# Kernel optimization log

Hardware: AMD Instinct MI355X
Metric: run time of the kernel (lower is better)

## Reference

```python
import jax, jax.numpy as jnp
import numpy as np

N_NODES = 50000
N_EDGES = 500000
IN_DIM = 64
OUT_DIM = 64
NUM_RELS = 16


def setup_inputs() -> dict:
    key = jax.random.key(0)
    ks = jax.random.split(key, 8)
    h = jax.random.normal(ks[0], (N_NODES, IN_DIM), dtype=jnp.float32)
    he = jax.random.normal(ks[1], (N_EDGES, IN_DIM), dtype=jnp.float32)
    src = jax.random.randint(ks[2], (N_EDGES,), 0, N_NODES)
    dst = jax.random.randint(ks[3], (N_EDGES,), 0, N_NODES)
    rel = jax.random.randint(ks[4], (N_EDGES,), 0, NUM_RELS)
    # xavier-ish scales
    W_shared = jax.random.normal(ks[5], (OUT_DIM, IN_DIM), dtype=jnp.float32) * (2.0 / (IN_DIM + OUT_DIM)) ** 0.5
    W_attn = jax.random.normal(ks[6], (1, 3 * OUT_DIM), dtype=jnp.float32) * (2.0 / (3 * OUT_DIM + 1)) ** 0.5
    W_rel = jax.random.normal(ks[7], (NUM_RELS, IN_DIM, OUT_DIM), dtype=jnp.float32) * (2.0 / (IN_DIM + OUT_DIM)) ** 0.5
    return {"h": h, "he": he, "src": src, "dst": dst, "rel": rel,
            "W_shared": W_shared, "W_attn": W_attn, "W_rel": W_rel}


def reference(h, he, src, dst, rel, W_shared, W_attn, W_rel):
    # --- edge attention: a = attn_fc([z_src, z_edge, z_dst]) (raw linear score, no softmax in original) ---
    Z = h @ W_shared.T                      # [N, out] project all nodes once
    ze = he @ W_shared.T                    # [E, out]
    # split attn weight to avoid materializing [E, 3*out] concat
    Wa_s, Wa_e, Wa_d = jnp.split(W_attn, 3, axis=1)   # each [1, out]
    a = Z[src] @ Wa_s.T + ze @ Wa_e.T + Z[dst] @ Wa_d.T   # [E, 1]
    # --- message: msg = (h_src @ W_rel[rel]) * a ---
    # compute per-(node, relation) transform once [N, R, out], then gather per edge
    H_all = jnp.einsum('ni,rio->nro', h, W_rel)          # [N, R, out]
    msg = H_all[src, rel] * a                             # [E, out]
    # --- scatter-sum aggregation into destination nodes ---
    out = jax.ops.segment_sum(msg, dst, num_segments=N_NODES)  # [N, out]
    # apply_func: activation (relu), no bias
    return jax.nn.relu(out)
```

## Files before the change

### kernel.cpp

```cpp
#include <hip/hip_runtime.h>
#include <math.h>

#define N_NODES 50000
#define N_EDGES 500000
#define NUM_RELS 16
#define GH 64
#define SCAN_BLKS 196
#define AE_BLKS 1954

typedef _Float16 f16x8 __attribute__((ext_vector_type(8)));
typedef _Float16 f16x4 __attribute__((ext_vector_type(4)));
typedef float    f32x4 __attribute__((ext_vector_type(4)));


__global__ void kz(int* __restrict__ c1, int* __restrict__ cu1,
                   int* __restrict__ c2, int* __restrict__ cu2) {
    int i = blockIdx.x * 256 + threadIdx.x;
    if (i < NUM_RELS) { c1[i] = 0; cu1[i] = 0; }
    if (i < N_NODES)  { c2[i] = 0; cu2[i] = 0; }
}

__global__ __launch_bounds__(256) void k_node(
    const float* __restrict__ h,
    const float* __restrict__ W_shared, const float* __restrict__ W_attn,
    const int* __restrict__ dst, const int* __restrict__ rel,
    float* __restrict__ sn, float* __restrict__ dn,
    int* __restrict__ c1, int* __restrict__ c2,
    _Float16* __restrict__ h_hi, _Float16* __restrict__ h_lo) {
    __shared__ float sus[64], sud[64];
    __shared__ int hist[NUM_RELS];
    const int t = threadIdx.x, bid = blockIdx.x, nb = gridDim.x;
    if (t < 64) {
        float us = 0.f, ud = 0.f;
        for (int o = 0; o < 64; ++o) {
            float w = W_shared[o * 64 + t];
            us = fmaf(w, W_attn[o],       us);
            ud = fmaf(w, W_attn[128 + o], ud);
        }
        sus[t] = us; sud[t] = ud;
    }
    if (t < NUM_RELS) hist[t] = 0;
    __syncthreads();

    int n = bid * 256 + t;
    if (n < N_NODES) {
        const float* hp = h + (size_t)n * 64;
        float s = 0.f, d = 0.f;
#pragma unroll
        for (int i = 0; i < 64; i += 4) {
            float4 v = *(const float4*)(hp + i);
            s = fmaf(v.x, sus[i], s);     s = fmaf(v.y, sus[i + 1], s);
            s = fmaf(v.z, sus[i + 2], s); s = fmaf(v.w, sus[i + 3], s);
            d = fmaf(v.x, sud[i], d);     d = fmaf(v.y, sud[i + 1], d);
            d = fmaf(v.z, sud[i + 2], d); d = fmaf(v.w, sud[i + 3], d);
            f16x4 hi, lo;
            hi[0] = (_Float16)v.x; lo[0] = (_Float16)(v.x - (float)hi[0]);
            hi[1] = (_Float16)v.y; lo[1] = (_Float16)(v.y - (float)hi[1]);
            hi[2] = (_Float16)v.z; lo[2] = (_Float16)(v.z - (float)hi[2]);
            hi[3] = (_Float16)v.w; lo[3] = (_Float16)(v.w - (float)hi[3]);
            *(f16x4*)(h_hi + (size_t)n * 64 + i) = hi;
            *(f16x4*)(h_lo + (size_t)n * 64 + i) = lo;
        }
        sn[n] = s; dn[n] = d;
    }
    for (int e = bid * 256 + t; e < N_EDGES; e += nb * 256) {
        atomicAdd(&hist[rel[e]], 1);
        atomicAdd(&c2[dst[e]], 1);
    }
    __syncthreads();
    if (t < NUM_RELS && hist[t]) atomicAdd(&c1[t], hist[t]);
}

__global__ __launch_bounds__(256) void k_scan1(const int* __restrict__ c2,
                                               int* __restrict__ partial) {
    const int t = threadIdx.x, bid = blockIdx.x;
    const int lane = t & 63, wv = t >> 6;
    __shared__ int ws[4];
    int idx = bid * 256 + t;
    int s = (idx < N_NODES) ? c2[idx] : 0;
#pragma unroll
    for (int off = 32; off > 0; off >>= 1) s += __shfl_xor(s, off, 64);
    if (lane == 0) ws[wv] = s;
    __syncthreads();
    if (t == 0) partial[bid] = ws[0] + ws[1] + ws[2] + ws[3];
}

__global__ __launch_bounds__(256) void k_scan2(const int* __restrict__ partial,
                                               int* __restrict__ pbase,
                                               int* __restrict__ offs2,
                                               const int* __restrict__ c1,
                                               int* __restrict__ offs1) {
    const int t = threadIdx.x;
    const int lane = t & 63, wv = t >> 6;
    __shared__ int wsum[4];
    int v = (t < SCAN_BLKS) ? partial[t] : 0;
    int x = v;
#pragma unroll
    for (int off = 1; off < 64; off <<= 1) {
        int y = __shfl_up(x, off, 64);
        if (lane >= off) x += y;
    }
    if (lane == 63) wsum[wv] = x;
    __syncthreads();
    int wbase = 0;
#pragma unroll
    for (int j = 0; j < 4; ++j) if (j < wv) wbase += wsum[j];
    int excl = wbase + x - v;
    pbase[t] = excl;
    if (t == 255) offs2[N_NODES] = excl;
    if (t == 0) {
        int b = 0;
        for (int r = 0; r < NUM_RELS; ++r) { offs1[r] = b; b += c1[r]; }
        offs1[NUM_RELS] = b;
    }
}

__global__ __launch_bounds__(256) void k_scan3(int* __restrict__ c2,
                                               const int* __restrict__ pbase,
                                               int* __restrict__ offs2) {
    const int t = threadIdx.x, bid = blockIdx.x;
    const int lane = t & 63, wv = t >> 6;
    __shared__ int wsum[4];
    int idx = bid * 256 + t;
    int v = (idx < N_NODES) ? c2[idx] : 0;
    int x = v;
#pragma unroll
    for (int off = 1; off < 64; off <<= 1) {
        int y = __shfl_up(x, off, 64);
        if (lane >= off) x += y;
    }
    if (lane == 63) wsum[wv] = x;
    __syncthreads();
    int wbase = 0;
#pragma unroll
    for (int j = 0; j < 4; ++j) if (j < wv) wbase += wsum[j];
    if (idx < N_NODES) offs2[idx] = pbase[bid] + wbase + x - v;
    if (idx < 4096) c2[idx] = 0;
}

__global__ __launch_bounds__(256) void k_ae(
    const float4* __restrict__ he4,
    const int* __restrict__ src, const int* __restrict__ dst,
    const int* __restrict__ rel,
    const float* __restrict__ W_shared, const float* __restrict__ W_attn,
    const float* __restrict__ sn, const float* __restrict__ dn,
    const int* __restrict__ offs1, int* __restrict__ cur1p,
    const int* __restrict__ offs2, int* __restrict__ cursor2,
    int* __restrict__ srcs, float* __restrict__ aes, int* __restrict__ iperm) {
    __shared__ float sve[64];
    __shared__ int hist[NUM_RELS], bbase[NUM_RELS], soffs[NUM_RELS];
    const int t = threadIdx.x;
    const int e = blockIdx.x * 256 + t;
    if (t < 64) {
        float ve = 0.f;
        for (int o = 0; o < 64; ++o)
            ve = fmaf(W_shared[o * 64 + t], W_attn[64 + o], ve);
        sve[t] = ve;
    }
    if (t < NUM_RELS) { hist[t] = 0; soffs[t] = offs1[t]; }
    const bool valid = (e < N_EDGES);
    int r = 0, s_ = 0, d_ = 0;
    float sdv = 0.f;
    if (valid) {
        s_ = src[e]; d_ = dst[e]; r = rel[e];
        sdv = sn[s_] + dn[d_];
    }
    __syncthreads();
    int lpos = 0; float aev = 0.f;
    if (valid) {
        const float4* hr = he4 + (size_t)e * 16;
        float acc = 0.f;
#pragma unroll
        for (int i = 0; i < 16; ++i) {
            float4 v = hr[i];
            float4 u = *(const float4*)(sve + 4 * i);
            acc += v.x * u.x + v.y * u.y + v.z * u.z + v.w * u.w;
        }
        aev = acc + sdv;
        lpos = atomicAdd(&hist[r], 1);
    }
    __syncthreads();
    if (t < NUM_RELS) bbase[t] = hist[t] ? atomicAdd(&cur1p[t << 8], hist[t]) : 0;
    __syncthreads();
    if (valid) {
        int p1 = soffs[r] + bbase[r] + lpos;
        srcs[p1] = s_; aes[p1] = aev;
        int p2 = offs2[d_] + atomicAdd(&cursor2[d_], 1);
        iperm[p2] = p1;
    }
}

__global__ __launch_bounds__(256, 4) void k_msg(
    const _Float16* __restrict__ h_hi, const _Float16* __restrict__ h_lo,
    const float* __restrict__ W_rel, const int* __restrict__ offs1,
    const int* __restrict__ srcs, const float* __restrict__ aes,
    float* __restrict__ msg)
{
    const int t = threadIdx.x;
    const int lane = t & 63;
    const int quad = lane >> 4;
    const int col  = lane & 15;
    const int wib  = t >> 6;
    const int rh   = blockIdx.x & 31;
    const int r    = rh & 15;
    const int half = rh >> 4;
    const int g    = blockIdx.x >> 5;
    const int wr   = g * 4 + wib;

    const int begin = __builtin_amdgcn_readfirstlane(offs1[r]);
    const int end   = __builtin_amdgcn_readfirstlane(offs1[r + 1]);

    const float* Wb = W_rel + (size_t)r * 4096;
    f16x8 bh[2][2], bl[2][2];
#pragma unroll
    for (int kb = 0; kb < 2; ++kb)
#pragma unroll
        for (int n2 = 0; n2 < 2; ++n2)
#pragma unroll
            for (int j = 0; j < 8; ++j) {
                float w = Wb[(kb * 32 + quad * 8 + j) * 64 + (half * 2 + n2) * 16 + col];
                _Float16 hi = (_Float16)w;
                bh[kb][n2][j] = hi;
                bl[kb][n2][j] = (_Float16)(w - (float)hi);
            }

    for (int base = begin + wr * 16; base < end; base += 256 * 16) {
        int m16 = end - base; if (m16 > 16) m16 = 16;
        const int ridx = base + (col < m16 ? col : m16 - 1);
        const int   sv = srcs[ridx];
        const float av = (col < m16) ? aes[ridx] : 0.f;

        const _Float16* ph = h_hi + (size_t)sv * 64 + quad * 8;
        const _Float16* pl = h_lo + (size_t)sv * 64 + quad * 8;
        f16x8 ah0 = *(const f16x8*)ph, ah1 = *(const f16x8*)(ph + 32);
        f16x8 al0 = *(const f16x8*)pl, al1 = *(const f16x8*)(pl + 32);

        f32x4 acc0 = {0.f, 0.f, 0.f, 0.f};
        f32x4 acc1 = {0.f, 0.f, 0.f, 0.f};
        acc0 = __builtin_amdgcn_mfma_f32_16x16x32_f16(ah0, bh[0][0], acc0, 0, 0, 0);
        acc1 = __builtin_amdgcn_mfma_f32_16x16x32_f16(ah0, bh[0][1], acc1, 0, 0, 0);
        acc0 = __builtin_amdgcn_mfma_f32_16x16x32_f16(ah0, bl[0][0], acc0, 0, 0, 0);
        acc1 = __builtin_amdgcn_mfma_f32_16x16x32_f16(ah0, bl[0][1], acc1, 0, 0, 0);
        acc0 = __builtin_amdgcn_mfma_f32_16x16x32_f16(al0, bh[0][0], acc0, 0, 0, 0);
        acc1 = __builtin_amdgcn_mfma_f32_16x16x32_f16(al0, bh[0][1], acc1, 0, 0, 0);
        acc0 = __builtin_amdgcn_mfma_f32_16x16x32_f16(ah1, bh[1][0], acc0, 0, 0, 0);
        acc1 = __builtin_amdgcn_mfma_f32_16x16x32_f16(ah1, bh[1][1], acc1, 0, 0, 0);
        acc0 = __builtin_amdgcn_mfma_f32_16x16x32_f16(ah1, bl[1][0], acc0, 0, 0, 0);
        acc1 = __builtin_amdgcn_mfma_f32_16x16x32_f16(ah1, bl[1][1], acc1, 0, 0, 0);
        acc0 = __builtin_amdgcn_mfma_f32_16x16x32_f16(al1, bh[1][0], acc0, 0, 0, 0);
        acc1 = __builtin_amdgcn_mfma_f32_16x16x32_f16(al1, bh[1][1], acc1, 0, 0, 0);

#pragma unroll
        for (int reg = 0; reg < 4; ++reg) {
            const int m = quad * 4 + reg;
            const float am = __shfl(av, m, 64);
            if (m < m16) {
                float* op = msg + (size_t)(base + m) * 64 + half * 32 + col;
                op[0]  = am * acc0[reg];
                op[16] = am * acc1[reg];
            }
        }
    }
}

__global__ __launch_bounds__(256) void k_out(
    const float* __restrict__ msg, const int* __restrict__ iperm,
    const int* __restrict__ offs2, float* __restrict__ out)
{
    const int lane = threadIdx.x & 63;
    const int gw   = blockIdx.x * 4 + (threadIdx.x >> 6);
    const int nw   = gridDim.x * 4;
    for (int n = gw; n < N_NODES; n += nw) {
        const int qb = offs2[n], qe = offs2[n + 1];
        float s0 = 0.f, s1 = 0.f, s2 = 0.f, s3 = 0.f;
        int q = qb;
        for (; q + 4 <= qe; q += 4) {
            int p0 = iperm[q], p1 = iperm[q + 1], p2 = iperm[q + 2], p3 = iperm[q + 3];
            s0 += msg[(size_t)p0 * 64 + lane];
            s1 += msg[(size_t)p1 * 64 + lane];
            s2 += msg[(size_t)p2 * 64 + lane];
            s3 += msg[(size_t)p3 * 64 + lane];
        }
        for (; q < qe; ++q)
            s0 += msg[(size_t)iperm[q] * 64 + lane];
        float s = (s0 + s1) + (s2 + s3);
        out[(size_t)n * 64 + lane] = fmaxf(s, 0.f);
    }
}

extern "C" void kernel_launch(void* const* d_in, const int* in_sizes, int n_in,
                              void* d_out, int out_size, void* d_ws, size_t ws_size,
                              hipStream_t stream) {
    const float*  h        = (const float*)d_in[0];
    const float4* he4      = (const float4*)d_in[1];
    const int*    src      = (const int*)d_in[2];
    const int*    dst      = (const int*)d_in[3];
    const int*    rel      = (const int*)d_in[4];
    const float*  W_shared = (const float*)d_in[5];
    const float*  W_attn   = (const float*)d_in[6];
    const float*  W_rel    = (const float*)d_in[7];
    float*        out      = (float*)d_out;

    int*      counts1 = (int*)d_ws + 0;
    int*      cursor1 = (int*)d_ws + 16;
    int*      offs1   = (int*)d_ws + 32;
    int*      counts2 = (int*)d_ws + 64;
    int*      cursor2 = (int*)d_ws + 50064;
    int*      offs2   = (int*)d_ws + 100064;
    float*    sn      = (float*)d_ws + 150080;
    float*    dn      = (float*)d_ws + 200080;
    int*      srcs    = (int*)d_ws + 250080;
    float*    aes     = (float*)d_ws + 750080;
    int*      iperm   = (int*)d_ws + 1250080;
    _Float16* h_hi    = (_Float16*)((int*)d_ws + 1750080);
    _Float16* h_lo    = (_Float16*)((int*)d_ws + 3350080);
    int*      partial = srcs;
    int*      pbase   = srcs + 256;
    float*    msg     = (float*)d_in[1];

    kz<<<(N_NODES + 255) / 256, 256, 0, stream>>>(counts1, cursor1, counts2, cursor2);
    k_node<<<196, 256, 0, stream>>>(h, W_shared, W_attn, dst, rel,
                                    sn, dn, counts1, counts2, h_hi, h_lo);
    k_scan1<<<SCAN_BLKS, 256, 0, stream>>>(counts2, partial);
    k_scan2<<<1, 256, 0, stream>>>(partial, pbase, offs2, counts1, offs1);
    k_scan3<<<SCAN_BLKS, 256, 0, stream>>>(counts2, pbase, offs2);
    k_ae<<<AE_BLKS, 256, 0, stream>>>(he4, src, dst, rel, W_shared, W_attn, sn, dn,
                                      offs1, counts2, offs2, cursor2, srcs, aes, iperm);
    k_msg<<<32 * GH, 256, 0, stream>>>(h_hi, h_lo, W_rel, offs1, srcs, aes, msg);
    k_out<<<2048, 256, 0, stream>>>(msg, iperm, offs2, out);
}
```

Baseline: 343.2 us.

## Coalesce edge-feature loads and scatter messages into destination order

k_ae now loads the edge-feature block cooperatively so consecutive lanes read consecutive float4s, computing per-edge dot products with shuffle reductions and shared memory. The permutation is inverted: k_msg writes each message directly to its destination-sorted slot, so k_out reads messages contiguously without an index gather. This trades gathered reads in the aggregation for scattered (but row-contiguous) writes in the message kernel, plus an extra perm load per edge.

```diff
diff --git a/kernel.cpp b/kernel.cpp
--- a/kernel.cpp
+++ b/kernel.cpp
@@ -146,11 +146,25 @@
     const float* __restrict__ sn, const float* __restrict__ dn,
     const int* __restrict__ offs1, int* __restrict__ cur1p,
     const int* __restrict__ offs2, int* __restrict__ cursor2,
-    int* __restrict__ srcs, float* __restrict__ aes, int* __restrict__ iperm) {
+    int* __restrict__ srcs, float* __restrict__ aes, int* __restrict__ perm) {
     __shared__ float sve[64];
+    __shared__ float sdot[256];
     __shared__ int hist[NUM_RELS], bbase[NUM_RELS], soffs[NUM_RELS];
     const int t = threadIdx.x;
+    const int lane = t & 63;
+    const int w = t >> 6;
     const int e = blockIdx.x * 256 + t;
+
+    const size_t fb = ((size_t)blockIdx.x * 256 + (size_t)w * 64) * 16;
+    const size_t fmax = (size_t)N_EDGES * 16 - 1;
+    float4 v[16];
+#pragma unroll
+    for (int k = 0; k < 16; ++k) {
+        size_t fi = fb + (size_t)k * 64 + lane;
+        if (fi > fmax) fi = fmax;
+        v[k] = he4[fi];
+    }
+
     if (t < 64) {
         float ve = 0.f;
         for (int o = 0; o < 64; ++o)
@@ -166,17 +180,22 @@
         sdv = sn[s_] + dn[d_];
     }
     __syncthreads();
+
+    {
+        float4 u = *(const float4*)(sve + 4 * (lane & 15));
+#pragma unroll
+        for (int k = 0; k < 16; ++k) {
+            float p = v[k].x * u.x + v[k].y * u.y + v[k].z * u.z + v[k].w * u.w;
+            p += __shfl_xor(p, 1, 64);
+            p += __shfl_xor(p, 2, 64);
+            p += __shfl_xor(p, 4, 64);
+            p += __shfl_xor(p, 8, 64);
+            if ((lane & 15) == 0) sdot[w * 64 + k * 4 + (lane >> 4)] = p;
+        }
+    }
     int lpos = 0; float aev = 0.f;
     if (valid) {
-        const float4* hr = he4 + (size_t)e * 16;
-        float acc = 0.f;
-#pragma unroll
-        for (int i = 0; i < 16; ++i) {
-            float4 v = hr[i];
-            float4 u = *(const float4*)(sve + 4 * i);
-            acc += v.x * u.x + v.y * u.y + v.z * u.z + v.w * u.w;
-        }
-        aev = acc + sdv;
+        aev = sdot[t] + sdv;
         lpos = atomicAdd(&hist[r], 1);
     }
     __syncthreads();
@@ -186,7 +205,7 @@
         int p1 = soffs[r] + bbase[r] + lpos;
         srcs[p1] = s_; aes[p1] = aev;
         int p2 = offs2[d_] + atomicAdd(&cursor2[d_], 1);
-        iperm[p2] = p1;
+        perm[p1] = p2;
     }
 }
 
@@ -194,7 +213,7 @@
     const _Float16* __restrict__ h_hi, const _Float16* __restrict__ h_lo,
     const float* __restrict__ W_rel, const int* __restrict__ offs1,
     const int* __restrict__ srcs, const float* __restrict__ aes,
-    float* __restrict__ msg)
+    const int* __restrict__ perm, float* __restrict__ msg)
 {
     const int t = threadIdx.x;
     const int lane = t & 63;
@@ -229,6 +248,7 @@
         const int ridx = base + (col < m16 ? col : m16 - 1);
         const int   sv = srcs[ridx];
         const float av = (col < m16) ? aes[ridx] : 0.f;
+        const int   pv = (col < m16) ? perm[ridx] : 0;
 
         const _Float16* ph = h_hi + (size_t)sv * 64 + quad * 8;
         const _Float16* pl = h_lo + (size_t)sv * 64 + quad * 8;
@@ -254,8 +274,9 @@
         for (int reg = 0; reg < 4; ++reg) {
             const int m = quad * 4 + reg;
             const float am = __shfl(av, m, 64);
+            const int   pm = __shfl(pv, m, 64);
             if (m < m16) {
-                float* op = msg + (size_t)(base + m) * 64 + half * 32 + col;
+                float* op = msg + (size_t)pm * 64 + half * 32 + col;
                 op[0]  = am * acc0[reg];
                 op[16] = am * acc1[reg];
             }
@@ -264,7 +285,7 @@
 }
 
 __global__ __launch_bounds__(256) void k_out(
-    const float* __restrict__ msg, const int* __restrict__ iperm,
+    const float* __restrict__ msg,
     const int* __restrict__ offs2, float* __restrict__ out)
 {
     const int lane = threadIdx.x & 63;
@@ -275,14 +296,13 @@
         float s0 = 0.f, s1 = 0.f, s2 = 0.f, s3 = 0.f;
         int q = qb;
         for (; q + 4 <= qe; q += 4) {
-            int p0 = iperm[q], p1 = iperm[q + 1], p2 = iperm[q + 2], p3 = iperm[q + 3];
-            s0 += msg[(size_t)p0 * 64 + lane];
-            s1 += msg[(size_t)p1 * 64 + lane];
-            s2 += msg[(size_t)p2 * 64 + lane];
-            s3 += msg[(size_t)p3 * 64 + lane];
+            s0 += msg[(size_t)q * 64 + lane];
+            s1 += msg[(size_t)(q + 1) * 64 + lane];
+            s2 += msg[(size_t)(q + 2) * 64 + lane];
+            s3 += msg[(size_t)(q + 3) * 64 + lane];
         }
         for (; q < qe; ++q)
-            s0 += msg[(size_t)iperm[q] * 64 + lane];
+            s0 += msg[(size_t)q * 64 + lane];
         float s = (s0 + s1) + (s2 + s3);
         out[(size_t)n * 64 + lane] = fmaxf(s, 0.f);
     }
@@ -311,7 +331,7 @@
     float*    dn      = (float*)d_ws + 200080;
     int*      srcs    = (int*)d_ws + 250080;
     float*    aes     = (float*)d_ws + 750080;
-    int*      iperm   = (int*)d_ws + 1250080;
+    int*      perm    = (int*)d_ws + 1250080;
     _Float16* h_hi    = (_Float16*)((int*)d_ws + 1750080);
     _Float16* h_lo    = (_Float16*)((int*)d_ws + 3350080);
     int*      partial = srcs;
@@ -325,7 +345,7 @@
     k_scan2<<<1, 256, 0, stream>>>(partial, pbase, offs2, counts1, offs1);
     k_scan3<<<SCAN_BLKS, 256, 0, stream>>>(counts2, pbase, offs2);
     k_ae<<<AE_BLKS, 256, 0, stream>>>(he4, src, dst, rel, W_shared, W_attn, sn, dn,
-                                      offs1, counts2, offs2, cursor2, srcs, aes, iperm);
-    k_msg<<<32 * GH, 256, 0, stream>>>(h_hi, h_lo, W_rel, offs1, srcs, aes, msg);
-    k_out<<<2048, 256, 0, stream>>>(msg, iperm, offs2, out);
-}
+                                      offs1, counts2, offs2, cursor2, srcs, aes, perm);
+    k_msg<<<32 * GH, 256, 0, stream>>>(h_hi, h_lo, W_rel, offs1, srcs, aes, perm, msg);
+    k_out<<<2048, 256, 0, stream>>>(msg, offs2, out);
+}
```

Result: no change. 337.8 us (-1.6%).

## Move edge-feature attention dot product into node kernel with coalesced wave loads

Applied to the files above, without the earlier changes.

The per-edge dot product of he with the folded attention vector moves out of k_ae into k_node. k_node now launches one block per 256 edges and reads he with coalesced wave-wide float4 loads, reducing with cross-lane shuffles, instead of one thread striding through its own 256-byte row. Node work and histogramming stay on the first SCAN_BLKS blocks. The cost is an extra edot buffer written and then reread in k_ae, plus 16 float4 registers per thread.

```diff
diff --git a/kernel.cpp b/kernel.cpp
--- a/kernel.cpp
+++ b/kernel.cpp
@@ -21,54 +21,88 @@
 }
 
 __global__ __launch_bounds__(256) void k_node(
-    const float* __restrict__ h,
+    const float* __restrict__ h, const float4* __restrict__ he4,
     const float* __restrict__ W_shared, const float* __restrict__ W_attn,
     const int* __restrict__ dst, const int* __restrict__ rel,
     float* __restrict__ sn, float* __restrict__ dn,
     int* __restrict__ c1, int* __restrict__ c2,
-    _Float16* __restrict__ h_hi, _Float16* __restrict__ h_lo) {
-    __shared__ float sus[64], sud[64];
+    _Float16* __restrict__ h_hi, _Float16* __restrict__ h_lo,
+    float* __restrict__ edot) {
+    __shared__ float sus[64], sud[64], sve[64];
+    __shared__ float sdot[256];
     __shared__ int hist[NUM_RELS];
-    const int t = threadIdx.x, bid = blockIdx.x, nb = gridDim.x;
+    const int t = threadIdx.x, bid = blockIdx.x;
+    const int lane = t & 63;
+    const int w = t >> 6;
+
+    const size_t fb = ((size_t)bid * 256 + (size_t)w * 64) * 16;
+    const size_t fmax = (size_t)N_EDGES * 16 - 1;
+    float4 v[16];
+#pragma unroll
+    for (int k = 0; k < 16; ++k) {
+        size_t fi = fb + (size_t)k * 64 + lane;
+        if (fi > fmax) fi = fmax;
+        v[k] = he4[fi];
+    }
+
     if (t < 64) {
-        float us = 0.f, ud = 0.f;
+        float us = 0.f, ud = 0.f, ve = 0.f;
         for (int o = 0; o < 64; ++o) {
-            float w = W_shared[o * 64 + t];
-            us = fmaf(w, W_attn[o],       us);
-            ud = fmaf(w, W_attn[128 + o], ud);
-        }
-        sus[t] = us; sud[t] = ud;
+            float ww = W_shared[o * 64 + t];
+            us = fmaf(ww, W_attn[o],       us);
+            ve = fmaf(ww, W_attn[64 + o],  ve);
+            ud = fmaf(ww, W_attn[128 + o], ud);
+        }
+        sus[t] = us; sud[t] = ud; sve[t] = ve;
     }
     if (t < NUM_RELS) hist[t] = 0;
     __syncthreads();
 
     int n = bid * 256 + t;
-    if (n < N_NODES) {
+    if (bid < SCAN_BLKS && n < N_NODES) {
         const float* hp = h + (size_t)n * 64;
         float s = 0.f, d = 0.f;
 #pragma unroll
         for (int i = 0; i < 64; i += 4) {
-            float4 v = *(const float4*)(hp + i);
-            s = fmaf(v.x, sus[i], s);     s = fmaf(v.y, sus[i + 1], s);
-            s = fmaf(v.z, sus[i + 2], s); s = fmaf(v.w, sus[i + 3], s);
-            d = fmaf(v.x, sud[i], d);     d = fmaf(v.y, sud[i + 1], d);
-            d = fmaf(v.z, sud[i + 2], d); d = fmaf(v.w, sud[i + 3], d);
+            float4 hv = *(const float4*)(hp + i);
+            s = fmaf(hv.x, sus[i], s);     s = fmaf(hv.y, sus[i + 1], s);
+            s = fmaf(hv.z, sus[i + 2], s); s = fmaf(hv.w, sus[i + 3], s);
+            d = fmaf(hv.x, sud[i], d);     d = fmaf(hv.y, sud[i + 1], d);
+            d = fmaf(hv.z, sud[i + 2], d); d = fmaf(hv.w, sud[i + 3], d);
             f16x4 hi, lo;
-            hi[0] = (_Float16)v.x; lo[0] = (_Float16)(v.x - (float)hi[0]);
-            hi[1] = (_Float16)v.y; lo[1] = (_Float16)(v.y - (float)hi[1]);
-            hi[2] = (_Float16)v.z; lo[2] = (_Float16)(v.z - (float)hi[2]);
-            hi[3] = (_Float16)v.w; lo[3] = (_Float16)(v.w - (float)hi[3]);
+            hi[0] = (_Float16)hv.x; lo[0] = (_Float16)(hv.x - (float)hi[0]);
+            hi[1] = (_Float16)hv.y; lo[1] = (_Float16)(hv.y - (float)hi[1]);
+            hi[2] = (_Float16)hv.z; lo[2] = (_Float16)(hv.z - (float)hi[2]);
+            hi[3] = (_Float16)hv.w; lo[3] = (_Float16)(hv.w - (float)hi[3]);
             *(f16x4*)(h_hi + (size_t)n * 64 + i) = hi;
             *(f16x4*)(h_lo + (size_t)n * 64 + i) = lo;
         }
         sn[n] = s; dn[n] = d;
     }
-    for (int e = bid * 256 + t; e < N_EDGES; e += nb * 256) {
-        atomicAdd(&hist[rel[e]], 1);
-        atomicAdd(&c2[dst[e]], 1);
-    }
-    __syncthreads();
-    if (t < NUM_RELS && hist[t]) atomicAdd(&c1[t], hist[t]);
+
+    {
+        float4 u = *(const float4*)(sve + 4 * (lane & 15));
+#pragma unroll
+        for (int k = 0; k < 16; ++k) {
+            float p = v[k].x * u.x + v[k].y * u.y + v[k].z * u.z + v[k].w * u.w;
+            p += __shfl_xor(p, 1, 64);
+            p += __shfl_xor(p, 2, 64);
+            p += __shfl_xor(p, 4, 64);
+            p += __shfl_xor(p, 8, 64);
+            if ((lane & 15) == 0) sdot[w * 64 + k * 4 + (lane >> 4)] = p;
+        }
+    }
+    int e = bid * 256 + t;
+    if (e < N_EDGES) edot[e] = sdot[t];
+
+    if (bid < SCAN_BLKS) {
+        for (int ee = bid * 256 + t; ee < N_EDGES; ee += SCAN_BLKS * 256) {
+            atomicAdd(&hist[rel[ee]], 1);
+            atomicAdd(&c2[dst[ee]], 1);
+        }
+    }
+    __syncthreads();
+    if (bid < SCAN_BLKS && t < NUM_RELS && hist[t]) atomicAdd(&c1[t], hist[t]);
 }
 
 __global__ __launch_bounds__(256) void k_scan1(const int* __restrict__ c2,
@@ -139,46 +173,26 @@
 }
 
 __global__ __launch_bounds__(256) void k_ae(
-    const float4* __restrict__ he4,
     const int* __restrict__ src, const int* __restrict__ dst,
-    const int* __restrict__ rel,
-    const float* __restrict__ W_shared, const float* __restrict__ W_attn,
+    const int* __restrict__ rel, const float* __restrict__ edot,
     const float* __restrict__ sn, const float* __restrict__ dn,
     const int* __restrict__ offs1, int* __restrict__ cur1p,
     const int* __restrict__ offs2, int* __restrict__ cursor2,
     int* __restrict__ srcs, float* __restrict__ aes, int* __restrict__ iperm) {
-    __shared__ float sve[64];
     __shared__ int hist[NUM_RELS], bbase[NUM_RELS], soffs[NUM_RELS];
     const int t = threadIdx.x;
     const int e = blockIdx.x * 256 + t;
-    if (t < 64) {
-        float ve = 0.f;
-        for (int o = 0; o < 64; ++o)
-            ve = fmaf(W_shared[o * 64 + t], W_attn[64 + o], ve);
-        sve[t] = ve;
-    }
     if (t < NUM_RELS) { hist[t] = 0; soffs[t] = offs1[t]; }
     const bool valid = (e < N_EDGES);
     int r = 0, s_ = 0, d_ = 0;
-    float sdv = 0.f;
+    float aev = 0.f;
     if (valid) {
         s_ = src[e]; d_ = dst[e]; r = rel[e];
-        sdv = sn[s_] + dn[d_];
-    }
-    __syncthreads();
-    int lpos = 0; float aev = 0.f;
-    if (valid) {
-        const float4* hr = he4 + (size_t)e * 16;
-        float acc = 0.f;
-#pragma unroll
-        for (int i = 0; i < 16; ++i) {
-            float4 v = hr[i];
-            float4 u = *(const float4*)(sve + 4 * i);
-            acc += v.x * u.x + v.y * u.y + v.z * u.z + v.w * u.w;
-        }
-        aev = acc + sdv;
-        lpos = atomicAdd(&hist[r], 1);
-    }
+        aev = edot[e] + sn[s_] + dn[d_];
+    }
+    __syncthreads();
+    int lpos = 0;
+    if (valid) lpos = atomicAdd(&hist[r], 1);
     __syncthreads();
     if (t < NUM_RELS) bbase[t] = hist[t] ? atomicAdd(&cur1p[t << 8], hist[t]) : 0;
     __syncthreads();
@@ -314,17 +328,18 @@
     int*      iperm   = (int*)d_ws + 1250080;
     _Float16* h_hi    = (_Float16*)((int*)d_ws + 1750080);
     _Float16* h_lo    = (_Float16*)((int*)d_ws + 3350080);
+    float*    edot    = (float*)d_ws + 4950080;
     int*      partial = srcs;
     int*      pbase   = srcs + 256;
     float*    msg     = (float*)d_in[1];
 
     kz<<<(N_NODES + 255) / 256, 256, 0, stream>>>(counts1, cursor1, counts2, cursor2);
-    k_node<<<196, 256, 0, stream>>>(h, W_shared, W_attn, dst, rel,
-                                    sn, dn, counts1, counts2, h_hi, h_lo);
+    k_node<<<AE_BLKS, 256, 0, stream>>>(h, he4, W_shared, W_attn, dst, rel,
+                                        sn, dn, counts1, counts2, h_hi, h_lo, edot);
     k_scan1<<<SCAN_BLKS, 256, 0, stream>>>(counts2, partial);
     k_scan2<<<1, 256, 0, stream>>>(partial, pbase, offs2, counts1, offs1);
     k_scan3<<<SCAN_BLKS, 256, 0, stream>>>(counts2, pbase, offs2);
-    k_ae<<<AE_BLKS, 256, 0, stream>>>(he4, src, dst, rel, W_shared, W_attn, sn, dn,
+    k_ae<<<AE_BLKS, 256, 0, stream>>>(src, dst, rel, edot, sn, dn,
                                       offs1, counts2, offs2, cursor2, srcs, aes, iperm);
     k_msg<<<32 * GH, 256, 0, stream>>>(h_hi, h_lo, W_rel, offs1, srcs, aes, msg);
     k_out<<<2048, 256, 0, stream>>>(msg, iperm, offs2, out);
```

New measurement: 356.3 us. 1.04x slower.
